# Kernel tuning notes

Hardware: AMD Instinct MI355X
Metric: run time of the kernel (lower is better)

Reference implementation:

```python
import jax, jax.numpy as jnp
import numpy as np

N = 50000      # num nodes
E = 1_600_000  # num edges
D = 64         # in_dim == hidden_dim
H = 4          # heads
C = 16         # head_dim = hidden_dim // heads
NEG = 0.2      # leaky_relu negative slope (PyG GATConv default)


def setup_inputs() -> dict:
    key = jax.random.key(0)
    ks = jax.random.split(key, 20)
    f = lambda k, s: (jax.random.normal(k, s, jnp.float32) * 0.1)
    return dict(
        node_features=jax.random.normal(ks[0], (N, D), jnp.float32),
        edge_index=jax.random.randint(ks[1], (2, E), 0, N, dtype=jnp.int32),
        edge_type=jax.random.randint(ks[2], (E,), 0, 5, dtype=jnp.int32),
        edge_attr=jax.random.normal(ks[3], (E, 1), jnp.float32),
        # GAT layer 1 (PyG GATConv: lin has no bias, att_* are [H,C], final bias [H*C])
        W1=f(ks[4], (D, H * C)), att_src1=f(ks[5], (H, C)), att_dst1=f(ks[6], (H, C)),
        We1=f(ks[7], (1, H * C)), att_e1=f(ks[8], (H, C)), b1=jnp.zeros((H * C,), jnp.float32),
        # GAT layer 2
        W2=f(ks[9], (D, H * C)), att_src2=f(ks[10], (H, C)), att_dst2=f(ks[11], (H, C)),
        We2=f(ks[12], (1, H * C)), att_e2=f(ks[13], (H, C)), b2=jnp.zeros((H * C,), jnp.float32),
        # LayerNorms
        g1=jnp.ones((D,), jnp.float32), beta1=jnp.zeros((D,), jnp.float32),
        g2=jnp.ones((D,), jnp.float32), beta2=jnp.zeros((D,), jnp.float32),
        # output head
        Wout=f(ks[14], (D, 1)), bout=jnp.zeros((1,), jnp.float32),
    )


def _layernorm(x, g, b, eps=1e-5):
    mu = x.mean(-1, keepdims=True)
    v = ((x - mu) ** 2).mean(-1, keepdims=True)
    return (x - mu) * jax.lax.rsqrt(v + eps) * g + b


def _seg_softmax(alpha, dst, n):
    # numerically stable segment softmax over incoming edges of each dst node
    m = jax.ops.segment_max(alpha, dst, num_segments=n)
    m = jnp.where(jnp.isfinite(m), m, 0.0)
    ex = jnp.exp(alpha - m[dst])
    den = jax.ops.segment_sum(ex, dst, num_segments=n)
    return ex / (den[dst] + 1e-16)


def _gatconv(x, src, dst, eattr, W, a_s, a_d, We, a_e, b, n):
    xs = (x @ W).reshape(n, H, C)                       # [N,H,C]
    a_src = jnp.einsum('nhc,hc->nh', xs, a_s)           # [N,H]
    a_dst = jnp.einsum('nhc,hc->nh', xs, a_d)           # [N,H]
    ee = (eattr @ We).reshape(-1, H, C)                 # [E',H,C]
    a_edge = jnp.einsum('ehc,hc->eh', ee, a_e)          # [E',H]
    alpha = a_src[src] + a_dst[dst] + a_edge            # [E',H]
    alpha = jax.nn.leaky_relu(alpha, NEG)
    alpha = _seg_softmax(alpha, dst, n)                 # [E',H]
    msg = xs[src] * alpha[..., None]                    # [E',H,C] gather-weighted messages
    out = jax.ops.segment_sum(msg, dst, num_segments=n) # scatter-aggregate
    return out.reshape(n, H * C) + b


def reference(node_features, edge_index, edge_type, edge_attr,
              W1, att_src1, att_dst1, We1, att_e1, b1,
              W2, att_src2, att_dst2, We2, att_e2, b2,
              g1, beta1, g2, beta2, Wout, bout):
    src, dst = edge_index[0], edge_index[1]
    # PyG add_self_loops(fill_value='mean'): self-loop edge_attr = mean of edge_attr over incoming edges
    cnt = jax.ops.segment_sum(jnp.ones((E,), jnp.float32), dst, num_segments=N)
    loop_attr = jax.ops.segment_sum(edge_attr, dst, num_segments=N) / jnp.maximum(cnt, 1.0)[:, None]
    loops = jnp.arange(N, dtype=src.dtype)
    src2 = jnp.concatenate([src, loops])
    dst2 = jnp.concatenate([dst, loops])
    ea = jnp.concatenate([edge_attr, loop_attr], axis=0)

    residual = node_features  # in_dim == hidden_dim -> no res_proj
    h = _gatconv(node_features, src2, dst2, ea, W1, att_src1, att_dst1, We1, att_e1, b1, N)
    h = jax.nn.elu(_layernorm(h + residual, g1, beta1))
    residual = h
    h = _gatconv(h, src2, dst2, ea, W2, att_src2, att_dst2, We2, att_e2, b2, N)
    h = jax.nn.elu(_layernorm(h + residual, g2, beta2))
    return h @ Wout + bout
```

## Files before the change

kernel.cpp:

```cpp
#include <hip/hip_runtime.h>
#include <hip/hip_bf16.h>
#include <cfloat>

#define NN 50000
#define NE 1600000
#define NEG 0.2f
#define NBKT 196
#define BNODE 256
#define P1_TILE 2048
#define P1_BLOCKS 782
#define GEMM_BLOCKS 782
#define BCAP 8704
#define SLOTS 96
#define L2E 1.4426950408889634f
#define SMEM_BYTES 10880

typedef __attribute__((ext_vector_type(8))) short bf8_t;
typedef __attribute__((ext_vector_type(4))) float f4_t;

__device__ __forceinline__ float bf16bits_to_f(unsigned v) {
  return __uint_as_float(v << 16);
}
__device__ __forceinline__ unsigned f_to_bf16bits(float f) {
  unsigned u = __float_as_uint(f);
  return (u + 0x7fffu + ((u >> 16) & 1u)) >> 16;
}

__device__ __forceinline__ bf8_t pack8(const float* p) {
  bf8_t r;
#pragma unroll
  for (int i = 0; i < 8; ++i) r[i] = (short)f_to_bf16bits(p[i]);
  return r;
}

__device__ void bin_body(char* smem, int blk, const int* __restrict__ src,
                         const int* __restrict__ dst,
                         const float* __restrict__ ea, int* __restrict__ gcnt,
                         int2* __restrict__ gbuf) {
  int* lcnt = (int*)smem;
  int* lcur = lcnt + NBKT;
  int t = threadIdx.x;
  if (t < NBKT) lcnt[t] = 0;
  __syncthreads();
  int e0 = blk * P1_TILE;
  int bb[8], vx[8], vy[8];
#pragma unroll
  for (int k = 0; k < 8; ++k) {
    int e = e0 + k * 256 + t;
    if (e < NE) {
      int d = dst[e];
      bb[k] = d >> 8;
      vx[k] = ((d & 255) << 16) | src[e];
      vy[k] = __float_as_int(ea[e]);
      atomicAdd(&lcnt[bb[k]], 1);
    } else {
      bb[k] = -1;
    }
  }
  __syncthreads();
  if (t < NBKT) lcur[t] = atomicAdd(&gcnt[t], lcnt[t]);
  __syncthreads();
#pragma unroll
  for (int k = 0; k < 8; ++k) {
    if (bb[k] >= 0) {
      int pos = atomicAdd(&lcur[bb[k]], 1);
      if (pos < BCAP) gbuf[(size_t)bb[k] * BCAP + pos] = make_int2(vx[k], vy[k]);
    }
  }
}

template <bool FP32IN>
__device__ void gemm_body(char* smem, int blk, const void* __restrict__ xin,
                          const float* __restrict__ W,
                          const float* __restrict__ att_s,
                          const float* __restrict__ att_d,
                          unsigned short* __restrict__ xsb,
                          float* __restrict__ a_src,
                          float* __restrict__ a_dst) {
  unsigned short(*Wt)[68] = (unsigned short(*)[68])smem;
  int t = threadIdx.x;
  for (int i = t; i < 4096; i += 256) {
    int k = i >> 6, n = i & 63;
    Wt[n][k] = (unsigned short)f_to_bf16bits(W[i]);
  }
  __syncthreads();
  {
    int k = t & 63, h = t >> 6;
    float ps = 0.f, pd = 0.f;
#pragma unroll
    for (int c = 0; c < 16; ++c) {
      float w = bf16bits_to_f(Wt[h * 16 + c][k]);
      ps = fmaf(w, att_s[h * 16 + c], ps);
      pd = fmaf(w, att_d[h * 16 + c], pd);
    }
    Wt[64 + h][k] = (unsigned short)f_to_bf16bits(ps * L2E);
    Wt[68 + h][k] = (unsigned short)f_to_bf16bits(pd * L2E);
    Wt[72 + h][k] = 0;
    Wt[76 + h][k] = 0;
  }
  __syncthreads();
  int lane = t & 63, wave = t >> 6;
  int quad = lane >> 4, n16 = lane & 15;

  bf8_t bfrag[5][2];
#pragma unroll
  for (int nt = 0; nt < 5; ++nt)
#pragma unroll
    for (int kk = 0; kk < 2; ++kk)
      bfrag[nt][kk] = *(const bf8_t*)&Wt[nt * 16 + n16][kk * 32 + quad * 8];

  int r0 = blk * 64 + wave * 16;
  int rowA = r0 + n16; if (rowA > NN - 1) rowA = NN - 1;
  bf8_t af0, af1;
  if (FP32IN) {
    const float* xr = (const float*)xin + (size_t)rowA * 64 + quad * 8;
    af0 = pack8(xr);
    af1 = pack8(xr + 32);
  } else {
    const bf8_t* xrow =
        (const bf8_t*)((const unsigned short*)xin + (size_t)rowA * 64);
    af0 = xrow[quad];
    af1 = xrow[4 + quad];
  }
#pragma unroll
  for (int nt = 0; nt < 5; ++nt) {
    f4_t acc = {0.f, 0.f, 0.f, 0.f};
    acc = __builtin_amdgcn_mfma_f32_16x16x32_bf16(af0, bfrag[nt][0], acc, 0, 0, 0);
    acc = __builtin_amdgcn_mfma_f32_16x16x32_bf16(af1, bfrag[nt][1], acc, 0, 0, 0);
    if (nt < 4) {
#pragma unroll
      for (int reg = 0; reg < 4; ++reg) {
        int row = r0 + quad * 4 + reg;
        if (row < NN)
          xsb[(size_t)row * 64 + nt * 16 + n16] =
              (unsigned short)f_to_bf16bits(acc[reg]);
      }
    } else {
#pragma unroll
      for (int reg = 0; reg < 4; ++reg) {
        int row = r0 + quad * 4 + reg;
        if (row < NN && n16 < 8) {
          if (n16 < 4) a_src[row * 4 + n16] = acc[reg];
          else a_dst[row * 4 + (n16 - 4)] = acc[reg];
        }
      }
    }
  }
}

__global__ __launch_bounds__(256) void front_kernel(
    const int* __restrict__ src, const int* __restrict__ dst,
    const float* __restrict__ ea, int* __restrict__ gcnt,
    int2* __restrict__ gbuf, const float* __restrict__ x,
    const float* __restrict__ W1, const float* __restrict__ as1,
    const float* __restrict__ ad1, unsigned short* __restrict__ xsb,
    float* __restrict__ a_src, float* __restrict__ a_dst) {
  __shared__ __align__(16) char smem[SMEM_BYTES];
  if (blockIdx.x < P1_BLOCKS) {
    bin_body(smem, blockIdx.x, src, dst, ea, gcnt, gbuf);
  } else {
    gemm_body<true>(smem, blockIdx.x - P1_BLOCKS, x, W1, as1, ad1, xsb, a_src,
                    a_dst);
  }
}

__global__ __launch_bounds__(256) void gemm2_kernel(
    const unsigned short* __restrict__ xin, const float* __restrict__ W,
    const float* __restrict__ att_s, const float* __restrict__ att_d,
    unsigned short* __restrict__ xsb, float* __restrict__ a_src,
    float* __restrict__ a_dst) {
  __shared__ __align__(16) char smem[SMEM_BYTES];
  gemm_body<false>(smem, blockIdx.x, xin, W, att_s, att_d, xsb, a_src, a_dst);
}

__global__ __launch_bounds__(1024) void build_kernel(
    const int* __restrict__ gcnt, const int2* __restrict__ gbuf,
    int* __restrict__ cnt, unsigned* __restrict__ csr) {
  __shared__ int lc[BNODE];
  int t = threadIdx.x;
  int b = blockIdx.x;
  if (t < BNODE) lc[t] = 0;
  __syncthreads();
  int len = gcnt[b]; if (len > BCAP) len = BCAP;
  const int2* buf = gbuf + (size_t)b * BCAP;
  for (int i = t; i < len; i += 1024) {
    int2 v = buf[i];
    int dl = (v.x >> 16) & 255;
    int s = v.x & 0xffff;
    int pos = atomicAdd(&lc[dl], 1);
    if (pos < SLOTS) {
      unsigned eb = ((unsigned)v.y) & 0xffff0000u;
      csr[(size_t)(b * BNODE + dl) * SLOTS + pos] = eb | (unsigned)s;
    }
  }
  __syncthreads();
  if (t < BNODE) {
    int n = b * BNODE + t;
    if (n < NN) cnt[n] = min(lc[t], SLOTS);
  }
}

template <bool HEAD>
__global__ __launch_bounds__(256) void aggregate_kernel(
    const int* __restrict__ cnt, const unsigned* __restrict__ csr,
    const unsigned short* __restrict__ xsb, const float* __restrict__ a_src,
    const float* __restrict__ a_dst, const float* __restrict__ We,
    const float* __restrict__ att_e, const float* __restrict__ bias,
    const void* __restrict__ resv, const float* __restrict__ g,
    const float* __restrict__ beta, const float* __restrict__ Wout,
    const float* __restrict__ bout, float* __restrict__ out,
    unsigned short* __restrict__ out_b) {
  __shared__ __align__(16) uint2 rec[4][64][4];
  int t = threadIdx.x;
  int lane = t & 63, wave = t >> 6;
  int half = lane >> 5;
  int d2 = lane & 31;
  int hb = d2 >> 3;
  int n = blockIdx.x * 8 + wave * 2 + half;

  float sp = We[lane] * att_e[lane];
#pragma unroll
  for (int off = 8; off; off >>= 1) sp += __shfl_xor(sp, off, 16);
  sp *= L2E;
  float s0 = __shfl(sp, 0, 64), s1 = __shfl(sp, 16, 64);
  float s2 = __shfl(sp, 32, 64), s3 = __shfl(sp, 48, 64);

  const float4 adv = *(const float4*)(a_dst + (size_t)n * 4);

  int dn = cnt[n];
  int mdn = max(dn, __shfl_xor(dn, 32, 64));
  float accx = 0.f, accy = 0.f, den = 0.f, easum = 0.f;
  const uint2* rpb = &rec[wave][half * 32][hb];
  const char* xd = (const char*)xsb + d2 * 4;

  for (int base = 0; base < mdn; base += 32) {
    int c = mdn - base; if (c > 32) c = 32;
    int el = base + d2;
    unsigned ce = (el < dn) ? csr[(size_t)n * SLOTS + el] : 0u;
    float ea = __uint_as_float(ce & 0xffff0000u);
    easum += ea;
    unsigned soff = (ce & 0xffffu) * 128u;
    float ex0 = 0.f, ex1 = 0.f, ex2 = 0.f, ex3 = 0.f;
    if (el < dn) {
      const float4 av = *(const float4*)(a_src + (size_t)(ce & 0xffffu) * 4);
      float a0 = av.x + fmaf(ea, s0, adv.x); a0 = fmaxf(a0, NEG * a0);
      float a1 = av.y + fmaf(ea, s1, adv.y); a1 = fmaxf(a1, NEG * a1);
      float a2 = av.z + fmaf(ea, s2, adv.z); a2 = fmaxf(a2, NEG * a2);
      float a3 = av.w + fmaf(ea, s3, adv.w); a3 = fmaxf(a3, NEG * a3);
      ex0 = exp2f(a0); ex1 = exp2f(a1); ex2 = exp2f(a2); ex3 = exp2f(a3);
    }
    uint4* wp = (uint4*)&rec[wave][lane][0];
    wp[0] = make_uint4(soff, __float_as_uint(ex0), soff, __float_as_uint(ex1));
    wp[1] = make_uint4(soff, __float_as_uint(ex2), soff, __float_as_uint(ex3));
    int c8 = (c + 3) & ~3;
    for (int j = 0; j < c8; j += 4) {
      uint2 va = rpb[(j + 0) * 4];
      uint2 vb = rpb[(j + 1) * 4];
      uint2 vc = rpb[(j + 2) * 4];
      uint2 vd = rpb[(j + 3) * 4];
      unsigned ua = *(const unsigned*)(xd + va.x);
      unsigned ub = *(const unsigned*)(xd + vb.x);
      unsigned uc = *(const unsigned*)(xd + vc.x);
      unsigned ud = *(const unsigned*)(xd + vd.x);
      float efa = __uint_as_float(va.y), efb = __uint_as_float(vb.y);
      float efc = __uint_as_float(vc.y), efd = __uint_as_float(vd.y);
      den += (efa + efb) + (efc + efd);
      accx = fmaf(efa, __uint_as_float(ua << 16), accx);
      accy = fmaf(efa, __uint_as_float(ua & 0xffff0000u), accy);
      accx = fmaf(efb, __uint_as_float(ub << 16), accx);
      accy = fmaf(efb, __uint_as_float(ub & 0xffff0000u), accy);
      accx = fmaf(efc, __uint_as_float(uc << 16), accx);
      accy = fmaf(efc, __uint_as_float(uc & 0xffff0000u), accy);
      accx = fmaf(efd, __uint_as_float(ud << 16), accx);
      accy = fmaf(efd, __uint_as_float(ud & 0xffff0000u), accy);
    }
  }

#pragma unroll
  for (int off = 16; off; off >>= 1) easum += __shfl_xor(easum, off, 32);

  float loop_ea = easum / fmaxf((float)dn, 1.0f);
  float as_h = a_src[(size_t)n * 4 + hb];
  float adn = (hb == 0) ? adv.x : (hb == 1) ? adv.y : (hb == 2) ? adv.z : adv.w;
  float sph = (hb == 0) ? s0 : (hb == 1) ? s1 : (hb == 2) ? s2 : s3;
  float a_self = as_h + fmaf(loop_ea, sph, adn);
  a_self = fmaxf(a_self, NEG * a_self);
  float ex_self = exp2f(a_self);
  den += ex_self;
  unsigned un = *(const unsigned*)((const char*)xsb + (size_t)n * 128 + d2 * 4);
  accx = fmaf(ex_self, __uint_as_float(un << 16), accx);
  accy = fmaf(ex_self, __uint_as_float(un & 0xffff0000u), accy);

  float rden = 1.f / (den + 1e-16f);
  const float2 bi = *(const float2*)(bias + d2 * 2);
  float2 rsd;
  if (HEAD) {
    unsigned ur =
        *(const unsigned*)((const unsigned short*)resv + (size_t)n * 64 + d2 * 2);
    rsd.x = bf16bits_to_f(ur & 0xffffu);
    rsd.y = __uint_as_float(ur & 0xffff0000u);
  } else {
    rsd = *(const float2*)((const float*)resv + (size_t)n * 64 + d2 * 2);
  }
  float vx = accx * rden + bi.x + rsd.x;
  float vy = accy * rden + bi.y + rsd.y;
  float s = vx + vy;
#pragma unroll
  for (int off = 16; off; off >>= 1) s += __shfl_xor(s, off, 32);
  float mu = s * (1.0f / 64.0f);
  float dx = vx - mu, dy = vy - mu;
  float var = dx * dx + dy * dy;
#pragma unroll
  for (int off = 16; off; off >>= 1) var += __shfl_xor(var, off, 32);
  var *= (1.0f / 64.0f);
  float rstd = rsqrtf(var + 1e-5f);
  const float2 gg = *(const float2*)(g + d2 * 2);
  const float2 bb = *(const float2*)(beta + d2 * 2);
  float yx = dx * rstd * gg.x + bb.x;
  float yy = dy * rstd * gg.y + bb.y;
  yx = yx > 0.f ? yx : expm1f(yx);
  yy = yy > 0.f ? yy : expm1f(yy);
  if (HEAD) {
    const float2 wv = *(const float2*)(Wout + d2 * 2);
    float p = yx * wv.x + yy * wv.y;
#pragma unroll
    for (int off = 16; off; off >>= 1) p += __shfl_xor(p, off, 32);
    if (d2 == 0) out[n] = p + bout[0];
  } else {
    unsigned ob = f_to_bf16bits(yx) | (f_to_bf16bits(yy) << 16);
    *(unsigned*)(out_b + (size_t)n * 64 + d2 * 2) = ob;
  }
}

extern "C" void kernel_launch(void* const* d_in, const int* in_sizes, int n_in,
                              void* d_out, int out_size, void* d_ws,
                              size_t ws_size, hipStream_t stream) {
  const float* node_features = (const float*)d_in[0];
  const int* edge_index = (const int*)d_in[1];
  const int* src = edge_index;
  const int* dst = edge_index + NE;
  const float* edge_attr = (const float*)d_in[3];
  const float* W1 = (const float*)d_in[4];
  const float* att_src1 = (const float*)d_in[5];
  const float* att_dst1 = (const float*)d_in[6];
  const float* We1 = (const float*)d_in[7];
  const float* att_e1 = (const float*)d_in[8];
  const float* b1 = (const float*)d_in[9];
  const float* W2 = (const float*)d_in[10];
  const float* att_src2 = (const float*)d_in[11];
  const float* att_dst2 = (const float*)d_in[12];
  const float* We2 = (const float*)d_in[13];
  const float* att_e2 = (const float*)d_in[14];
  const float* b2 = (const float*)d_in[15];
  const float* g1 = (const float*)d_in[16];
  const float* beta1 = (const float*)d_in[17];
  const float* g2 = (const float*)d_in[18];
  const float* beta2 = (const float*)d_in[19];
  const float* Wout = (const float*)d_in[20];
  const float* bout = (const float*)d_in[21];
  float* out = (float*)d_out;

  char* ws = (char*)d_ws;
  size_t o = 0;
  auto alloc = [&](size_t bytes) {
    void* p = ws + o;
    o += (bytes + 255) & ~(size_t)255;
    return p;
  };
  int* gcnt = (int*)alloc((size_t)NBKT * 4);
  int2* gbuf = (int2*)alloc((size_t)NBKT * BCAP * 8);
  int* cnt = (int*)alloc((size_t)NN * 4);
  unsigned* csr = (unsigned*)alloc((size_t)NN * SLOTS * 4);
  unsigned short* xsb = (unsigned short*)alloc((size_t)NN * 64 * 2);
  unsigned short* h1b = (unsigned short*)alloc((size_t)NN * 64 * 2);
  float* a_srcb = (float*)alloc((size_t)NN * 4 * 4);
  float* a_dstb = (float*)alloc((size_t)NN * 4 * 4);

  hipMemsetAsync(gcnt, 0, (size_t)NBKT * 4, stream);

  front_kernel<<<P1_BLOCKS + GEMM_BLOCKS, 256, 0, stream>>>(
      src, dst, edge_attr, gcnt, gbuf, node_features, W1, att_src1, att_dst1,
      xsb, a_srcb, a_dstb);
  build_kernel<<<NBKT, 1024, 0, stream>>>(gcnt, gbuf, cnt, csr);

  aggregate_kernel<false><<<NN / 8, 256, 0, stream>>>(
      cnt, csr, xsb, a_srcb, a_dstb, We1, att_e1, b1, node_features, g1, beta1,
      nullptr, nullptr, nullptr, h1b);

  gemm2_kernel<<<GEMM_BLOCKS, 256, 0, stream>>>(h1b, W2, att_src2, att_dst2,
                                                xsb, a_srcb, a_dstb);
  aggregate_kernel<true><<<NN / 8, 256, 0, stream>>>(
      cnt, csr, xsb, a_srcb, a_dstb, We2, att_e2, b2, h1b, g2, beta2, Wout,
      bout, out, nullptr);
}
```

Baseline: 239.2 us.

## Vectorize edge binning loads, double rows per GEMM block, unroll gather by 8

The edge binning pass now has each thread read 8 consecutive edges with int4 vector loads instead of strided scalar loads. The GEMM blocks each process two 64-row sets, which halves the block count and amortizes the weight-fragment setup. The aggregation gather loop is unrolled to 8 neighbors per iteration to raise memory-level parallelism. The risks are more padded iterations on low-degree nodes, and edge order within a bucket changes, which alters the floating-point summation order.

```diff
diff --git a/kernel.cpp b/kernel.cpp
--- a/kernel.cpp
+++ b/kernel.cpp
@@ -9,7 +9,7 @@
 #define BNODE 256
 #define P1_TILE 2048
 #define P1_BLOCKS 782
-#define GEMM_BLOCKS 782
+#define GEMM_BLOCKS 391
 #define BCAP 8704
 #define SLOTS 96
 #define L2E 1.4426950408889634f
@@ -42,19 +42,36 @@
   int t = threadIdx.x;
   if (t < NBKT) lcnt[t] = 0;
   __syncthreads();
-  int e0 = blk * P1_TILE;
+  int e0 = blk * P1_TILE + t * 8;
   int bb[8], vx[8], vy[8];
-#pragma unroll
-  for (int k = 0; k < 8; ++k) {
-    int e = e0 + k * 256 + t;
-    if (e < NE) {
-      int d = dst[e];
-      bb[k] = d >> 8;
-      vx[k] = ((d & 255) << 16) | src[e];
-      vy[k] = __float_as_int(ea[e]);
+  if (e0 + 8 <= NE) {
+    int4 d0 = *(const int4*)(dst + e0), d1 = *(const int4*)(dst + e0 + 4);
+    int4 s0 = *(const int4*)(src + e0), s1 = *(const int4*)(src + e0 + 4);
+    int4 a0 = *(const int4*)((const int*)ea + e0);
+    int4 a1 = *(const int4*)((const int*)ea + e0 + 4);
+    int dd[8] = {d0.x, d0.y, d0.z, d0.w, d1.x, d1.y, d1.z, d1.w};
+    int ss[8] = {s0.x, s0.y, s0.z, s0.w, s1.x, s1.y, s1.z, s1.w};
+    int aa[8] = {a0.x, a0.y, a0.z, a0.w, a1.x, a1.y, a1.z, a1.w};
+#pragma unroll
+    for (int k = 0; k < 8; ++k) {
+      bb[k] = dd[k] >> 8;
+      vx[k] = ((dd[k] & 255) << 16) | ss[k];
+      vy[k] = aa[k];
       atomicAdd(&lcnt[bb[k]], 1);
-    } else {
-      bb[k] = -1;
+    }
+  } else {
+#pragma unroll
+    for (int k = 0; k < 8; ++k) {
+      int e = e0 + k;
+      if (e < NE) {
+        int d = dst[e];
+        bb[k] = d >> 8;
+        vx[k] = ((d & 255) << 16) | src[e];
+        vy[k] = __float_as_int(ea[e]);
+        atomicAdd(&lcnt[bb[k]], 1);
+      } else {
+        bb[k] = -1;
+      }
     }
   }
   __syncthreads();
@@ -109,39 +126,42 @@
     for (int kk = 0; kk < 2; ++kk)
       bfrag[nt][kk] = *(const bf8_t*)&Wt[nt * 16 + n16][kk * 32 + quad * 8];
 
-  int r0 = blk * 64 + wave * 16;
-  int rowA = r0 + n16; if (rowA > NN - 1) rowA = NN - 1;
-  bf8_t af0, af1;
-  if (FP32IN) {
-    const float* xr = (const float*)xin + (size_t)rowA * 64 + quad * 8;
-    af0 = pack8(xr);
-    af1 = pack8(xr + 32);
-  } else {
-    const bf8_t* xrow =
-        (const bf8_t*)((const unsigned short*)xin + (size_t)rowA * 64);
-    af0 = xrow[quad];
-    af1 = xrow[4 + quad];
-  }
-#pragma unroll
-  for (int nt = 0; nt < 5; ++nt) {
-    f4_t acc = {0.f, 0.f, 0.f, 0.f};
-    acc = __builtin_amdgcn_mfma_f32_16x16x32_bf16(af0, bfrag[nt][0], acc, 0, 0, 0);
-    acc = __builtin_amdgcn_mfma_f32_16x16x32_bf16(af1, bfrag[nt][1], acc, 0, 0, 0);
-    if (nt < 4) {
-#pragma unroll
-      for (int reg = 0; reg < 4; ++reg) {
-        int row = r0 + quad * 4 + reg;
-        if (row < NN)
-          xsb[(size_t)row * 64 + nt * 16 + n16] =
-              (unsigned short)f_to_bf16bits(acc[reg]);
-      }
+#pragma unroll
+  for (int set = 0; set < 2; ++set) {
+    int r0 = blk * 128 + set * 64 + wave * 16;
+    int rowA = r0 + n16; if (rowA > NN - 1) rowA = NN - 1;
+    bf8_t af0, af1;
+    if (FP32IN) {
+      const float* xr = (const float*)xin + (size_t)rowA * 64 + quad * 8;
+      af0 = pack8(xr);
+      af1 = pack8(xr + 32);
     } else {
-#pragma unroll
-      for (int reg = 0; reg < 4; ++reg) {
-        int row = r0 + quad * 4 + reg;
-        if (row < NN && n16 < 8) {
-          if (n16 < 4) a_src[row * 4 + n16] = acc[reg];
-          else a_dst[row * 4 + (n16 - 4)] = acc[reg];
+      const bf8_t* xrow =
+          (const bf8_t*)((const unsigned short*)xin + (size_t)rowA * 64);
+      af0 = xrow[quad];
+      af1 = xrow[4 + quad];
+    }
+#pragma unroll
+    for (int nt = 0; nt < 5; ++nt) {
+      f4_t acc = {0.f, 0.f, 0.f, 0.f};
+      acc = __builtin_amdgcn_mfma_f32_16x16x32_bf16(af0, bfrag[nt][0], acc, 0, 0, 0);
+      acc = __builtin_amdgcn_mfma_f32_16x16x32_bf16(af1, bfrag[nt][1], acc, 0, 0, 0);
+      if (nt < 4) {
+#pragma unroll
+        for (int reg = 0; reg < 4; ++reg) {
+          int row = r0 + quad * 4 + reg;
+          if (row < NN)
+            xsb[(size_t)row * 64 + nt * 16 + n16] =
+                (unsigned short)f_to_bf16bits(acc[reg]);
+        }
+      } else {
+#pragma unroll
+        for (int reg = 0; reg < 4; ++reg) {
+          int row = r0 + quad * 4 + reg;
+          if (row < NN && n16 < 8) {
+            if (n16 < 4) a_src[row * 4 + n16] = acc[reg];
+            else a_dst[row * 4 + (n16 - 4)] = acc[reg];
+          }
         }
       }
     }
@@ -252,27 +272,45 @@
     uint4* wp = (uint4*)&rec[wave][lane][0];
     wp[0] = make_uint4(soff, __float_as_uint(ex0), soff, __float_as_uint(ex1));
     wp[1] = make_uint4(soff, __float_as_uint(ex2), soff, __float_as_uint(ex3));
-    int c8 = (c + 3) & ~3;
-    for (int j = 0; j < c8; j += 4) {
-      uint2 va = rpb[(j + 0) * 4];
-      uint2 vb = rpb[(j + 1) * 4];
-      uint2 vc = rpb[(j + 2) * 4];
-      uint2 vd = rpb[(j + 3) * 4];
-      unsigned ua = *(const unsigned*)(xd + va.x);
-      unsigned ub = *(const unsigned*)(xd + vb.x);
-      unsigned uc = *(const unsigned*)(xd + vc.x);
-      unsigned ud = *(const unsigned*)(xd + vd.x);
-      float efa = __uint_as_float(va.y), efb = __uint_as_float(vb.y);
-      float efc = __uint_as_float(vc.y), efd = __uint_as_float(vd.y);
-      den += (efa + efb) + (efc + efd);
-      accx = fmaf(efa, __uint_as_float(ua << 16), accx);
-      accy = fmaf(efa, __uint_as_float(ua & 0xffff0000u), accy);
-      accx = fmaf(efb, __uint_as_float(ub << 16), accx);
-      accy = fmaf(efb, __uint_as_float(ub & 0xffff0000u), accy);
-      accx = fmaf(efc, __uint_as_float(uc << 16), accx);
-      accy = fmaf(efc, __uint_as_float(uc & 0xffff0000u), accy);
-      accx = fmaf(efd, __uint_as_float(ud << 16), accx);
-      accy = fmaf(efd, __uint_as_float(ud & 0xffff0000u), accy);
+    int c8 = (c + 7) & ~7;
+    for (int j = 0; j < c8; j += 8) {
+      uint2 v0 = rpb[(j + 0) * 4];
+      uint2 v1 = rpb[(j + 1) * 4];
+      uint2 v2 = rpb[(j + 2) * 4];
+      uint2 v3 = rpb[(j + 3) * 4];
+      uint2 v4 = rpb[(j + 4) * 4];
+      uint2 v5 = rpb[(j + 5) * 4];
+      uint2 v6 = rpb[(j + 6) * 4];
+      uint2 v7 = rpb[(j + 7) * 4];
+      unsigned u0 = *(const unsigned*)(xd + v0.x);
+      unsigned u1 = *(const unsigned*)(xd + v1.x);
+      unsigned u2 = *(const unsigned*)(xd + v2.x);
+      unsigned u3 = *(const unsigned*)(xd + v3.x);
+      unsigned u4 = *(const unsigned*)(xd + v4.x);
+      unsigned u5 = *(const unsigned*)(xd + v5.x);
+      unsigned u6 = *(const unsigned*)(xd + v6.x);
+      unsigned u7 = *(const unsigned*)(xd + v7.x);
+      float e0f = __uint_as_float(v0.y), e1f = __uint_as_float(v1.y);
+      float e2f = __uint_as_float(v2.y), e3f = __uint_as_float(v3.y);
+      float e4f = __uint_as_float(v4.y), e5f = __uint_as_float(v5.y);
+      float e6f = __uint_as_float(v6.y), e7f = __uint_as_float(v7.y);
+      den += ((e0f + e1f) + (e2f + e3f)) + ((e4f + e5f) + (e6f + e7f));
+      accx = fmaf(e0f, __uint_as_float(u0 << 16), accx);
+      accy = fmaf(e0f, __uint_as_float(u0 & 0xffff0000u), accy);
+      accx = fmaf(e1f, __uint_as_float(u1 << 16), accx);
+      accy = fmaf(e1f, __uint_as_float(u1 & 0xffff0000u), accy);
+      accx = fmaf(e2f, __uint_as_float(u2 << 16), accx);
+      accy = fmaf(e2f, __uint_as_float(u2 & 0xffff0000u), accy);
+      accx = fmaf(e3f, __uint_as_float(u3 << 16), accx);
+      accy = fmaf(e3f, __uint_as_float(u3 & 0xffff0000u), accy);
+      accx = fmaf(e4f, __uint_as_float(u4 << 16), accx);
+      accy = fmaf(e4f, __uint_as_float(u4 & 0xffff0000u), accy);
+      accx = fmaf(e5f, __uint_as_float(u5 << 16), accx);
+      accy = fmaf(e5f, __uint_as_float(u5 & 0xffff0000u), accy);
+      accx = fmaf(e6f, __uint_as_float(u6 << 16), accx);
+      accy = fmaf(e6f, __uint_as_float(u6 & 0xffff0000u), accy);
+      accx = fmaf(e7f, __uint_as_float(u7 << 16), accx);
+      accy = fmaf(e7f, __uint_as_float(u7 & 0xffff0000u), accy);
     }
   }
 
```

Measured after the change: 236.0 us. About the same (-1.3%).
